# Kernel optimization log

Hardware: AMD Instinct MI355X
Metric: run time of the kernel (lower is better)

Reference implementation:

```python
import jax, jax.numpy as jnp
import numpy as np

# Fixed query graph: 3 terms, 3 predicates, edges (head_term, tail_term, pred):
# (0,1,0), (1,2,1), (0,2,2) -> every term has degree 2 -> seq_len 3 incl. self.
T, P, B, D, H, NL, FF = 3, 3, 16384, 256, 8, 2, 1024
DH = D // H
SCALE = DH ** -0.5


def setup_inputs() -> dict:
    key = jax.random.key(0)
    ks = jax.random.split(key, 8)
    s = 0.02
    f = jnp.float32
    return {
        "term_embs": jax.random.normal(ks[0], (T, B, D), f),
        "pred_embs": jax.random.normal(ks[1], (P, B, D), f),
        "Wq": jax.random.normal(ks[2], (NL, D, D), f) * s,
        "Wk": jax.random.normal(ks[3], (NL, D, D), f) * s,
        "Wv": jax.random.normal(ks[4], (NL, D, D), f) * s,
        "Wo": jax.random.normal(ks[5], (NL, D, D), f) * s,
        "bq": jnp.zeros((NL, D), f),
        "bk": jnp.zeros((NL, D), f),
        "bv": jnp.zeros((NL, D), f),
        "bo": jnp.zeros((NL, D), f),
        "ln1_g": jnp.ones((NL, D), f),
        "ln1_b": jnp.zeros((NL, D), f),
        "ln2_g": jnp.ones((NL, D), f),
        "ln2_b": jnp.zeros((NL, D), f),
        "W1": jax.random.normal(ks[6], (NL, D, FF), f) * s,
        "b1": jnp.zeros((NL, FF), f),
        "W2": jax.random.normal(ks[7], (NL, FF, D), f) * s,
        "b2": jnp.zeros((NL, D), f),
        "lnf_g": jnp.ones((D,), f),
        "lnf_b": jnp.zeros((D,), f),
    }


def _layer_norm(x, g, b):
    m = jnp.mean(x, axis=-1, keepdims=True)
    v = jnp.var(x, axis=-1, keepdims=True)
    return (x - m) * jax.lax.rsqrt(v + 1e-5) * g + b


def _forward(term_embs, pred_embs, Wq, Wk, Wv, Wo, bq, bk, bv, bo,
             ln1_g, ln1_b, ln2_g, ln2_b, W1, b1, W2, b2, lnf_g, lnf_b):
    # --- message passing (TransE-style NBP): tail_est = head + pred, head_est = tail - pred
    # edge heads: [0,1,0], edge tails: [1,2,2]
    tail_msgs = term_embs[jnp.array([0, 1, 0])] + pred_embs  # [P,B,D] -> sent to tail terms
    head_msgs = term_embs[jnp.array([1, 2, 2])] - pred_embs  # [P,B,D] -> sent to head terms
    # collect per term (static gather) + self embedding appended last
    x0 = jnp.stack([head_msgs[0], head_msgs[2], term_embs[0]], axis=1)  # [B,3,D]
    x1 = jnp.stack([tail_msgs[0], head_msgs[1], term_embs[1]], axis=1)
    x2 = jnp.stack([tail_msgs[1], tail_msgs[2], term_embs[2]], axis=1)
    x = jnp.concatenate([x0, x1, x2], axis=0)  # [T*B, 3, D]
    # --- pre-norm Transformer encoder, NL layers (dropout off at eval)
    for l in range(NL):
        h = _layer_norm(x, ln1_g[l], ln1_b[l])
        q = (h @ Wq[l] + bq[l]).reshape(-1, 3, H, DH)
        k = (h @ Wk[l] + bk[l]).reshape(-1, 3, H, DH)
        v = (h @ Wv[l] + bv[l]).reshape(-1, 3, H, DH)
        a = jax.nn.softmax(jnp.einsum('nqhd,nkhd->nhqk', q, k) * SCALE, axis=-1)
        o = jnp.einsum('nhqk,nkhd->nqhd', a, v).reshape(-1, 3, D)
        x = x + o @ Wo[l] + bo[l]
        h = _layer_norm(x, ln2_g[l], ln2_b[l])
        x = x + jax.nn.relu(h @ W1[l] + b1[l]) @ W2[l] + b2[l]
    x = _layer_norm(x, lnf_g, lnf_b)
    # --- aggregate (agg_func='mean') over the small message sequence
    return jnp.mean(x, axis=1).reshape(T, B, D)


def reference(term_embs, pred_embs, Wq, Wk, Wv, Wo, bq, bk, bv, bo,
              ln1_g, ln1_b, ln2_g, ln2_b, W1, b1, W2, b2, lnf_g, lnf_b):
    return _forward(term_embs, pred_embs, Wq, Wk, Wv, Wo, bq, bk, bv, bo,
                    ln1_g, ln1_b, ln2_g, ln2_b, W1, b1, W2, b2, lnf_g, lnf_b)
```

## Files before the change

kernel.cpp:

```cpp
#include <hip/hip_runtime.h>
#include <hip/hip_bf16.h>
#include <stdint.h>

typedef __hip_bfloat16 bf16;
typedef unsigned short u16;
typedef unsigned int u32;
typedef __bf16 v8bf __attribute__((ext_vector_type(8)));
typedef float v4f __attribute__((ext_vector_type(4)));

#define NB 16384
#define MROWS 147456

__device__ __forceinline__ float b2f(u16 u) {
  union { u32 u; float f; } v; v.u = ((u32)u) << 16; return v.f;
}
__device__ __forceinline__ u16 f2b(float f) {
  union { float f; u32 u; } v; v.f = f;
  u32 u = v.u;
  return (u16)((u + 0x7fffu + ((u >> 16) & 1u)) >> 16);
}
__device__ __forceinline__ void async16(const u16* g, u16* lds) {
  __builtin_amdgcn_global_load_lds((const __attribute__((address_space(1))) void*)g,
                                   (__attribute__((address_space(3))) void*)lds,
                                   16, 0, 0);
}

__global__ __launch_bounds__(256)
void prep_weights(const float* Wq, const float* Wk, const float* Wv, const float* Wo,
                  const float* W1, const float* W2,
                  const float* bq, const float* bk, const float* bv,
                  bf16* wt, float* bqkv)
{
  if (blockIdx.x == 6144) {
    for (int e = threadIdx.x; e < 1536; e += 256) {
      int l = e / 768;
      int rem = e - l * 768;
      int wsel = rem >> 8;
      int col = rem & 255;
      const float* s = (wsel == 0) ? bq : (wsel == 1) ? bk : bv;
      bqkv[e] = s[l * 256 + col];
    }
    return;
  }
  int gid = blockIdx.x * 256 + threadIdx.x;
  int layer = (gid >= 786432) ? 1 : 0;
  int r = gid - layer * 786432;
  const float* src; int K, N, e, outoff;
  if (r < 262144) {
    int which = r >> 16;
    e = r & 65535; K = 256; N = 256;
    const float* w = (which == 0) ? Wq : (which == 1) ? Wk : (which == 2) ? Wv : Wo;
    src = w + layer * 65536;
    outoff = layer * 786432 + which * 65536;
  } else if (r < 524288) {
    e = r - 262144; K = 256; N = 1024;
    src = W1 + layer * 262144;
    outoff = layer * 786432 + 262144;
  } else {
    e = r - 524288; K = 1024; N = 256;
    src = W2 + layer * 262144;
    outoff = layer * 786432 + 524288;
  }
  int n = e / K, kk = e - n * K;
  ((u16*)wt)[outoff + e] = f2b(src[kk * N + n]);
}

__global__ __launch_bounds__(256)
void build_x(const float* __restrict__ T, const float* __restrict__ P,
             float* __restrict__ X, int row0)
{
  int tid = blockIdx.x * 256 + threadIdx.x;
  int lrow = tid >> 6;
  int d0 = (tid & 63) * 4;
  int row = row0 + lrow;
  int n = row / 3;
  int t = row - n * 3;
  size_t xoff = (size_t)lrow * 256 + d0;
  if (t == 2) {
    *(float4*)(X + xoff) = *(const float4*)(T + (size_t)n * 256 + d0);
    return;
  }
  int tm = n >> 14, b = n & 16383;
  const int srcT[6] = {1, 2,  0, 2,  1, 0};
  const int srcP[6] = {0, 2,  0, 1,  1, 2};
  const float sg[6] = {-1.f, -1.f,  1.f, -1.f,  1.f, 1.f};
  int idx = tm * 2 + t;
  float4 tv = *(const float4*)(T + ((size_t)(srcT[idx] * NB + b)) * 256 + d0);
  float4 pv = *(const float4*)(P + ((size_t)(srcP[idx] * NB + b)) * 256 + d0);
  float s = sg[idx];
  float4 ov;
  ov.x = tv.x + s * pv.x;
  ov.y = tv.y + s * pv.y;
  ov.z = tv.z + s * pv.z;
  ov.w = tv.w + s * pv.w;
  *(float4*)(X + xoff) = ov;
}

__global__ __launch_bounds__(256)
void ln_rows(const float* __restrict__ xp, const float* __restrict__ gp,
             const float* __restrict__ bp, bf16* __restrict__ hp)
{
  const int lane = threadIdx.x & 63;
  const int row = blockIdx.x * 4 + (threadIdx.x >> 6);
  float4 rv = *(const float4*)(xp + (size_t)row * 256 + lane * 4);
  float v0 = rv.x, v1 = rv.y, v2 = rv.z, v3 = rv.w;
  float s = v0 + v1 + v2 + v3;
  float q = v0 * v0 + v1 * v1 + v2 * v2 + v3 * v3;
  #pragma unroll
  for (int m = 32; m > 0; m >>= 1) {
    s += __shfl_xor(s, m, 64);
    q += __shfl_xor(q, m, 64);
  }
  float mean = s * (1.f / 256.f);
  float var = q * (1.f / 256.f) - mean * mean;
  float r = rsqrtf(var + 1e-5f);
  float4 gv = *(const float4*)(gp + lane * 4);
  float4 bv = *(const float4*)(bp + lane * 4);
  ushort4 outv;
  outv.x = f2b((v0 - mean) * r * gv.x + bv.x);
  outv.y = f2b((v1 - mean) * r * gv.y + bv.y);
  outv.z = f2b((v2 - mean) * r * gv.z + bv.z);
  outv.w = f2b((v3 - mean) * r * gv.w + bv.w);
  *(ushort4*)((u16*)hp + (size_t)row * 256 + lane * 4) = outv;
}

template<int RES, int RELU, int OUTF32>
__global__ __launch_bounds__(256)
void gemm_bt(const bf16* __restrict__ Ap, const bf16* __restrict__ Btp,
             const float* __restrict__ biasp, const float* __restrict__ resp,
             void* __restrict__ Cp, int N, int K,
             int btZ, int biasZ, long long cZ)
{
  __shared__ __align__(16) u16 As[128 * 32];
  __shared__ __align__(16) u16 Bs[128 * 32];
  const int z = blockIdx.z;
  const u16* A = (const u16*)Ap;
  const u16* Bt = (const u16*)Btp + (size_t)z * btZ;
  const float* bias = biasp + (size_t)z * biasZ;
  const int m0 = blockIdx.x * 128;
  const int n0 = blockIdx.y * 128;
  const int tid = threadIdx.x;
  const int w = tid >> 6, lane = tid & 63;
  const int waveM = (w & 1) * 64, waveN = (w >> 1) * 64;

  const int rrow = tid >> 2;
  const int kcol = (tid & 3) * 8;
  const u16* pA0 = A + (size_t)(m0 + rrow) * K + kcol;
  const u16* pA1 = A + (size_t)(m0 + rrow + 64) * K + kcol;
  const u16* pB0 = Bt + (size_t)(n0 + rrow) * K + kcol;
  const u16* pB1 = Bt + (size_t)(n0 + rrow + 64) * K + kcol;
  u16* lA0 = As + w * 512;
  u16* lA1 = As + 2048 + w * 512;
  u16* lB0 = Bs + w * 512;
  u16* lB1 = Bs + 2048 + w * 512;

  v4f acc[4][4];
  #pragma unroll
  for (int i = 0; i < 4; i++)
    #pragma unroll
    for (int j = 0; j < 4; j++) {
      v4f zz = {0.f, 0.f, 0.f, 0.f};
      acc[i][j] = zz;
    }

  const char* AsC = (const char*)As;
  const char* BsC = (const char*)Bs;
  const int rdA = (waveM + (lane & 15)) * 64 + (lane >> 4) * 16;
  const int rdB = (waveN + (lane & 15)) * 64 + (lane >> 4) * 16;

  for (int kt = 0; kt < K; kt += 32) {
    __syncthreads();
    async16(pA0, lA0); async16(pA1, lA1);
    async16(pB0, lB0); async16(pB1, lB1);
    pA0 += 32; pA1 += 32; pB0 += 32; pB1 += 32;
    __syncthreads();
    v8bf a[4], b[4];
    #pragma unroll
    for (int i = 0; i < 4; i++)
      a[i] = *(const v8bf*)(AsC + rdA + i * 1024);
    #pragma unroll
    for (int j = 0; j < 4; j++)
      b[j] = *(const v8bf*)(BsC + rdB + j * 1024);
    #pragma unroll
    for (int i = 0; i < 4; i++)
      #pragma unroll
      for (int j = 0; j < 4; j++)
        acc[i][j] = __builtin_amdgcn_mfma_f32_16x16x32_bf16(a[i], b[j], acc[i][j], 0, 0, 0);
  }

  float bv[4];
  #pragma unroll
  for (int j = 0; j < 4; j++)
    bv[j] = bias[n0 + waveN + j * 16 + (lane & 15)];

  #pragma unroll
  for (int i = 0; i < 4; i++) {
    #pragma unroll
    for (int r = 0; r < 4; r++) {
      int rowg = m0 + waveM + i * 16 + (lane >> 4) * 4 + r;
      size_t rb = (size_t)rowg * N;
      #pragma unroll
      for (int j = 0; j < 4; j++) {
        int colg = n0 + waveN + j * 16 + (lane & 15);
        float vv = acc[i][j][r] + bv[j];
        if (RES) vv += resp[rb + colg];
        if (RELU) vv = fmaxf(vv, 0.f);
        if (OUTF32) ((float*)Cp)[rb + colg] = vv;
        else ((u16*)Cp + (size_t)z * cZ)[rb + colg] = f2b(vv);
      }
    }
  }
}

__global__ __launch_bounds__(256)
void attn(const bf16* __restrict__ qp, const bf16* __restrict__ kp,
          const bf16* __restrict__ vp, bf16* __restrict__ op)
{
  __shared__ __align__(16) u16 qs[6144], ks[6144], vs[6144];
  __shared__ float probs[8][8][9];
  const int tid = threadIdx.x;
  const size_t gbase = (size_t)blockIdx.x * 6144;
  const uint4* qg = (const uint4*)((const u16*)qp + gbase);
  const uint4* kg = (const uint4*)((const u16*)kp + gbase);
  const uint4* vg = (const uint4*)((const u16*)vp + gbase);
  for (int c = tid; c < 768; c += 256) {
    ((uint4*)qs)[c] = qg[c];
    ((uint4*)ks)[c] = kg[c];
    ((uint4*)vs)[c] = vg[c];
  }
  __syncthreads();
  if (tid < 64) {
    int s = tid >> 3, h = tid & 7;
    int base = s * 768 + h * 32;
    float sc[3][3];
    #pragma unroll
    for (int i = 0; i < 3; i++)
      #pragma unroll
      for (int j = 0; j < 3; j++) {
        float sum = 0.f;
        #pragma unroll
        for (int d = 0; d < 32; d++)
          sum += b2f(qs[base + i * 256 + d]) * b2f(ks[base + j * 256 + d]);
        sc[i][j] = sum * 0.17677669529663687f;
      }
    #pragma unroll
    for (int i = 0; i < 3; i++) {
      float m = fmaxf(sc[i][0], fmaxf(sc[i][1], sc[i][2]));
      float e0 = __expf(sc[i][0] - m);
      float e1 = __expf(sc[i][1] - m);
      float e2 = __expf(sc[i][2] - m);
      float inv = 1.f / (e0 + e1 + e2);
      probs[s][h][i * 3 + 0] = e0 * inv;
      probs[s][h][i * 3 + 1] = e1 * inv;
      probs[s][h][i * 3 + 2] = e2 * inv;
    }
  }
  __syncthreads();
  u16* og = (u16*)op + gbase;
  for (int c = tid; c < 6144; c += 256) {
    int lrow = c >> 8, hd = c & 255;
    int s = lrow / 3, i = lrow - s * 3;
    int h = hd >> 5;
    float p0 = probs[s][h][i * 3 + 0];
    float p1 = probs[s][h][i * 3 + 1];
    float p2 = probs[s][h][i * 3 + 2];
    float o = p0 * b2f(vs[s * 768 + hd])
            + p1 * b2f(vs[s * 768 + 256 + hd])
            + p2 * b2f(vs[s * 768 + 512 + hd]);
    og[c] = f2b(o);
  }
}

__global__ __launch_bounds__(256)
void ln_final_mean(const float* __restrict__ xp, const float* __restrict__ gp,
                   const float* __restrict__ bp, float* __restrict__ outp)
{
  const int lane = threadIdx.x & 63;
  const int n = blockIdx.x * 4 + (threadIdx.x >> 6);
  float4 gv = *(const float4*)(gp + lane * 4);
  float4 bv4 = *(const float4*)(bp + lane * 4);
  float a0 = 0.f, a1 = 0.f, a2 = 0.f, a3 = 0.f;
  for (int t = 0; t < 3; t++) {
    float4 rv = *(const float4*)(xp + ((size_t)n * 3 + t) * 256 + lane * 4);
    float v0 = rv.x, v1 = rv.y, v2 = rv.z, v3 = rv.w;
    float s = v0 + v1 + v2 + v3;
    float q = v0 * v0 + v1 * v1 + v2 * v2 + v3 * v3;
    #pragma unroll
    for (int m = 32; m > 0; m >>= 1) {
      s += __shfl_xor(s, m, 64);
      q += __shfl_xor(q, m, 64);
    }
    float mean = s * (1.f / 256.f);
    float var = q * (1.f / 256.f) - mean * mean;
    float r = rsqrtf(var + 1e-5f);
    a0 += (v0 - mean) * r * gv.x + bv4.x;
    a1 += (v1 - mean) * r * gv.y + bv4.y;
    a2 += (v2 - mean) * r * gv.z + bv4.z;
    a3 += (v3 - mean) * r * gv.w + bv4.w;
  }
  const float third = 1.f / 3.f;
  float4 outv;
  outv.x = a0 * third;
  outv.y = a1 * third;
  outv.z = a2 * third;
  outv.w = a3 * third;
  *(float4*)(outp + (size_t)n * 256 + lane * 4) = outv;
}

extern "C" void kernel_launch(void* const* d_in, const int* in_sizes, int n_in,
                              void* d_out, int out_size, void* d_ws, size_t ws_size,
                              hipStream_t stream)
{
  const float* term = (const float*)d_in[0];
  const float* pred = (const float*)d_in[1];
  const float* Wq  = (const float*)d_in[2];
  const float* Wk  = (const float*)d_in[3];
  const float* Wv  = (const float*)d_in[4];
  const float* Wo  = (const float*)d_in[5];
  const float* bq  = (const float*)d_in[6];
  const float* bk  = (const float*)d_in[7];
  const float* bvv = (const float*)d_in[8];
  const float* bo  = (const float*)d_in[9];
  const float* ln1g = (const float*)d_in[10];
  const float* ln1b = (const float*)d_in[11];
  const float* ln2g = (const float*)d_in[12];
  const float* ln2b = (const float*)d_in[13];
  const float* W1  = (const float*)d_in[14];
  const float* b1  = (const float*)d_in[15];
  const float* W2  = (const float*)d_in[16];
  const float* b2  = (const float*)d_in[17];
  const float* lnfg = (const float*)d_in[18];
  const float* lnfb = (const float*)d_in[19];

  int nch = 128;
  for (int c = 1; c <= 128; c *= 2) {
    size_t Mc = (size_t)MROWS / c;
    size_t need = 4ull * 1024 * 1024 + Mc * 3584ull;
    if (need <= ws_size) { nch = c; break; }
  }
  const size_t Mc = (size_t)MROWS / nch;
  const int mBlocks = (int)(Mc / 128);

  char* ws = (char*)d_ws;
  bf16* wt   = (bf16*)ws;
  float* bqkv = (float*)(ws + 3145728);
  float* x = (float*)(ws + 4194304);
  bf16* h = (bf16*)(x + Mc * 256);
  bf16* q = h + Mc * 256;
  bf16* v_ = q + 2 * Mc * 256;
  bf16* o = q + 3 * Mc * 256;
  bf16* f = q;

  prep_weights<<<6145, 256, 0, stream>>>(Wq, Wk, Wv, Wo, W1, W2, bq, bk, bvv, wt, bqkv);

  const long long qkvZ = (long long)(Mc * 256);
  for (int ch = 0; ch < nch; ch++) {
    const int row0 = (int)(ch * Mc);
    build_x<<<(int)(Mc / 4), 256, 0, stream>>>(term, pred, x, row0);
    for (int l = 0; l < 2; l++) {
      const bf16* wl = wt + l * 786432;
      ln_rows<<<(int)(Mc / 4), 256, 0, stream>>>(x, ln1g + l * 256, ln1b + l * 256, h);
      gemm_bt<0, 0, 0><<<dim3(mBlocks, 2, 3), 256, 0, stream>>>(
          h, wl, bqkv + l * 768, nullptr, q, 256, 256, 65536, 256, qkvZ);
      attn<<<(int)(Mc / 24), 256, 0, stream>>>(q, q + Mc * 256, v_, o);
      gemm_bt<1, 0, 1><<<dim3(mBlocks, 2, 1), 256, 0, stream>>>(
          o, wl + 196608, bo + l * 256, x, x, 256, 256, 0, 0, 0);
      ln_rows<<<(int)(Mc / 4), 256, 0, stream>>>(x, ln2g + l * 256, ln2b + l * 256, h);
      gemm_bt<0, 1, 0><<<dim3(mBlocks, 8, 1), 256, 0, stream>>>(
          h, wl + 262144, b1 + l * 1024, nullptr, f, 1024, 256, 0, 0, 0);
      gemm_bt<1, 0, 1><<<dim3(mBlocks, 2, 1), 256, 0, stream>>>(
          f, wl + 524288, b2 + l * 256, x, x, 256, 1024, 0, 0, 0);
    }
    ln_final_mean<<<(int)(Mc / 12), 256, 0, stream>>>(
        x, lnfg, lnfb, (float*)d_out + (size_t)(row0 / 3) * 256);
  }
}
```

Measured before the change: 1.660 ms.

## Double-buffer GEMM LDS tiles and fuse input build with first layernorm

The GEMM main loop now uses two LDS buffers, so the async global-to-LDS loads for the next K tile are issued before the MFMAs on the current tile, with one barrier per iteration instead of two. The message-passing input construction is fused with the layer-0 pre-attention layernorm, removing one kernel launch and one read of the residual buffer. The cost is twice the LDS per GEMM block, which may reduce occupancy. The overlap may also be lost if the compiler inserts conservative waits on the async loads.

```diff
diff --git a/kernel.cpp b/kernel.cpp
--- a/kernel.cpp
+++ b/kernel.cpp
@@ -66,34 +66,52 @@
 }
 
 __global__ __launch_bounds__(256)
-void build_x(const float* __restrict__ T, const float* __restrict__ P,
-             float* __restrict__ X, int row0)
-{
-  int tid = blockIdx.x * 256 + threadIdx.x;
-  int lrow = tid >> 6;
-  int d0 = (tid & 63) * 4;
-  int row = row0 + lrow;
+void build_ln(const float* __restrict__ T, const float* __restrict__ P,
+              const float* __restrict__ gp, const float* __restrict__ bp,
+              float* __restrict__ X, bf16* __restrict__ H, int row0)
+{
+  const int lane = threadIdx.x & 63;
+  const int lrow = blockIdx.x * 4 + (threadIdx.x >> 6);
+  const int row = row0 + lrow;
+  const int d0 = lane * 4;
   int n = row / 3;
   int t = row - n * 3;
-  size_t xoff = (size_t)lrow * 256 + d0;
+  float4 v;
   if (t == 2) {
-    *(float4*)(X + xoff) = *(const float4*)(T + (size_t)n * 256 + d0);
-    return;
-  }
-  int tm = n >> 14, b = n & 16383;
-  const int srcT[6] = {1, 2,  0, 2,  1, 0};
-  const int srcP[6] = {0, 2,  0, 1,  1, 2};
-  const float sg[6] = {-1.f, -1.f,  1.f, -1.f,  1.f, 1.f};
-  int idx = tm * 2 + t;
-  float4 tv = *(const float4*)(T + ((size_t)(srcT[idx] * NB + b)) * 256 + d0);
-  float4 pv = *(const float4*)(P + ((size_t)(srcP[idx] * NB + b)) * 256 + d0);
-  float s = sg[idx];
-  float4 ov;
-  ov.x = tv.x + s * pv.x;
-  ov.y = tv.y + s * pv.y;
-  ov.z = tv.z + s * pv.z;
-  ov.w = tv.w + s * pv.w;
-  *(float4*)(X + xoff) = ov;
+    v = *(const float4*)(T + (size_t)n * 256 + d0);
+  } else {
+    int tm = n >> 14, b = n & 16383;
+    const int srcT[6] = {1, 2,  0, 2,  1, 0};
+    const int srcP[6] = {0, 2,  0, 1,  1, 2};
+    const float sg[6] = {-1.f, -1.f,  1.f, -1.f,  1.f, 1.f};
+    int idx = tm * 2 + t;
+    float4 tv = *(const float4*)(T + ((size_t)(srcT[idx] * NB + b)) * 256 + d0);
+    float4 pv = *(const float4*)(P + ((size_t)(srcP[idx] * NB + b)) * 256 + d0);
+    float s = sg[idx];
+    v.x = tv.x + s * pv.x;
+    v.y = tv.y + s * pv.y;
+    v.z = tv.z + s * pv.z;
+    v.w = tv.w + s * pv.w;
+  }
+  *(float4*)(X + (size_t)lrow * 256 + d0) = v;
+  float s = v.x + v.y + v.z + v.w;
+  float q = v.x * v.x + v.y * v.y + v.z * v.z + v.w * v.w;
+  #pragma unroll
+  for (int m = 32; m > 0; m >>= 1) {
+    s += __shfl_xor(s, m, 64);
+    q += __shfl_xor(q, m, 64);
+  }
+  float mean = s * (1.f / 256.f);
+  float var = q * (1.f / 256.f) - mean * mean;
+  float r = rsqrtf(var + 1e-5f);
+  float4 gv = *(const float4*)(gp + d0);
+  float4 bv = *(const float4*)(bp + d0);
+  ushort4 outv;
+  outv.x = f2b((v.x - mean) * r * gv.x + bv.x);
+  outv.y = f2b((v.y - mean) * r * gv.y + bv.y);
+  outv.z = f2b((v.z - mean) * r * gv.z + bv.z);
+  outv.w = f2b((v.w - mean) * r * gv.w + bv.w);
+  *(ushort4*)((u16*)H + (size_t)lrow * 256 + d0) = outv;
 }
 
 __global__ __launch_bounds__(256)
@@ -131,8 +149,8 @@
              void* __restrict__ Cp, int N, int K,
              int btZ, int biasZ, long long cZ)
 {
-  __shared__ __align__(16) u16 As[128 * 32];
-  __shared__ __align__(16) u16 Bs[128 * 32];
+  __shared__ __align__(16) u16 As[2 * 128 * 32];
+  __shared__ __align__(16) u16 Bs[2 * 128 * 32];
   const int z = blockIdx.z;
   const u16* A = (const u16*)Ap;
   const u16* Bt = (const u16*)Btp + (size_t)z * btZ;
@@ -149,10 +167,6 @@
   const u16* pA1 = A + (size_t)(m0 + rrow + 64) * K + kcol;
   const u16* pB0 = Bt + (size_t)(n0 + rrow) * K + kcol;
   const u16* pB1 = Bt + (size_t)(n0 + rrow + 64) * K + kcol;
-  u16* lA0 = As + w * 512;
-  u16* lA1 = As + 2048 + w * 512;
-  u16* lB0 = Bs + w * 512;
-  u16* lB1 = Bs + 2048 + w * 512;
 
   v4f acc[4][4];
   #pragma unroll
@@ -163,17 +177,25 @@
       acc[i][j] = zz;
     }
 
-  const char* AsC = (const char*)As;
-  const char* BsC = (const char*)Bs;
   const int rdA = (waveM + (lane & 15)) * 64 + (lane >> 4) * 16;
   const int rdB = (waveN + (lane & 15)) * 64 + (lane >> 4) * 16;
-
-  for (int kt = 0; kt < K; kt += 32) {
+  const int nk = K >> 5;
+
+  async16(pA0, As + w * 512);        async16(pA1, As + 2048 + w * 512);
+  async16(pB0, Bs + w * 512);        async16(pB1, Bs + 2048 + w * 512);
+  pA0 += 32; pA1 += 32; pB0 += 32; pB1 += 32;
+
+  int cur = 0;
+  for (int kt = 0; kt < nk; kt++) {
     __syncthreads();
-    async16(pA0, lA0); async16(pA1, lA1);
-    async16(pB0, lB0); async16(pB1, lB1);
-    pA0 += 32; pA1 += 32; pB0 += 32; pB1 += 32;
-    __syncthreads();
+    if (kt + 1 < nk) {
+      const int nxt = (cur ^ 1) * 4096;
+      async16(pA0, As + nxt + w * 512);        async16(pA1, As + nxt + 2048 + w * 512);
+      async16(pB0, Bs + nxt + w * 512);        async16(pB1, Bs + nxt + 2048 + w * 512);
+      pA0 += 32; pA1 += 32; pB0 += 32; pB1 += 32;
+    }
+    const char* AsC = (const char*)(As + cur * 4096);
+    const char* BsC = (const char*)(Bs + cur * 4096);
     v8bf a[4], b[4];
     #pragma unroll
     for (int i = 0; i < 4; i++)
@@ -186,6 +208,7 @@
       #pragma unroll
       for (int j = 0; j < 4; j++)
         acc[i][j] = __builtin_amdgcn_mfma_f32_16x16x32_bf16(a[i], b[j], acc[i][j], 0, 0, 0);
+    cur ^= 1;
   }
 
   float bv[4];
@@ -356,10 +379,11 @@
   const long long qkvZ = (long long)(Mc * 256);
   for (int ch = 0; ch < nch; ch++) {
     const int row0 = (int)(ch * Mc);
-    build_x<<<(int)(Mc / 4), 256, 0, stream>>>(term, pred, x, row0);
+    build_ln<<<(int)(Mc / 4), 256, 0, stream>>>(term, pred, ln1g, ln1b, x, h, row0);
     for (int l = 0; l < 2; l++) {
       const bf16* wl = wt + l * 786432;
-      ln_rows<<<(int)(Mc / 4), 256, 0, stream>>>(x, ln1g + l * 256, ln1b + l * 256, h);
+      if (l > 0)
+        ln_rows<<<(int)(Mc / 4), 256, 0, stream>>>(x, ln1g + l * 256, ln1b + l * 256, h);
       gemm_bt<0, 0, 0><<<dim3(mBlocks, 2, 3), 256, 0, stream>>>(
           h, wl, bqkv + l * 768, nullptr, q, 256, 256, 65536, 256, qkvZ);
       attn<<<(int)(Mc / 24), 256, 0, stream>>>(q, q + Mc * 256, v_, o);
```

Measured after the change: 1.592 ms. 4.1% less time.
